# Performance work log

Measured on AMD Instinct MI355X. Metric: run time of the kernel, lower is better.

The kernel has to match this reference:

```python
import jax, jax.numpy as jnp
import numpy as np


def setup_inputs() -> dict:
    key = jax.random.key(0)
    k1, k2 = jax.random.split(key, 2)
    B, C, N, O, K = 4, 3, 8192, 64, 20
    x = jax.random.normal(k1, (B, C, N), dtype=jnp.float32)          # point cloud [B,3,N]
    W = jax.random.normal(k2, (O, 2 * C), dtype=jnp.float32) * 0.1   # 1x1 conv weight on 2C edge features
    b = jnp.zeros((O,), dtype=jnp.float32)
    return {"x": x, "W": W, "b": b, "k": K}


def _knn_idx(x, k):
    # x: [B, C, N]. Same math as torch knn(): pd = -||xi||^2 + 2 xi.xj - ||xj||^2,
    # topk of pd (largest) == k nearest neighbors.
    inner = -2.0 * jnp.einsum('bcn,bcm->bnm', x, x)      # [B,N,N]
    xx = jnp.sum(x * x, axis=1)                          # [B,N]
    pd = -xx[:, :, None] - inner - xx[:, None, :]        # [B,N,N] negative sq-dist
    _, idx = jax.lax.top_k(pd, k)                        # [B,N,k]
    return idx


def reference(x, W, b, k):
    # Faithful jax version of knn + get_graph_feature + 1x1 conv + LeakyReLU + max over k
    # (DGCNN EdgeConv layer, the hot path of the encoder).
    B, C, N = x.shape
    idx = _knn_idx(x, k)                                  # [B,N,k]
    xt = jnp.transpose(x, (0, 2, 1))                      # [B,N,C]
    nb = xt[jnp.arange(B)[:, None, None], idx]            # gather neighbors [B,N,k,C]
    cen = xt[:, :, None, :]                               # [B,N,1,C]
    feat = jnp.concatenate(
        [nb - cen, jnp.broadcast_to(cen, (B, N, k, C))], axis=-1)  # [B,N,k,2C]
    h = jnp.einsum('bnkc,oc->bonk', feat, W) + b[None, :, None, None]  # [B,O,N,k]
    h = jax.nn.leaky_relu(h, negative_slope=0.2)
    return jnp.max(h, axis=-1)                            # [B,O,N]
```

## Files before the change

### kernel.cpp

```cpp
#include <hip/hip_runtime.h>
#include <cstdint>
#include <climits>

#pragma clang fp contract(off)

#define N_PTS 8192
#define B_SZ  4
#define K_NN  20
#define O_CH  64
#define QW    64
#define SSUB  8
#define JSUB  (N_PTS / SSUB)
#define WARM  64
#define CAP   16
#define SPAD  17

typedef unsigned long long u64k;

__device__ __forceinline__ float pd_np(float qx, float qy, float qz, float xxn,
                                       float cx, float cy, float cz, float xm) {
  float p0 = qx * cx;
  float p1 = qy * cy;
  float p2 = qz * cz;
  float dot = (p0 + p1) + p2;
  float t = 2.0f * dot - xxn;
  return t - xm;
}

__device__ __forceinline__ void insert20(float (&arr)[K_NN], float v) {
  float c = v;
#pragma unroll
  for (int u = K_NN - 1; u >= 0; --u) {
    float hi = fmaxf(arr[u], c);
    c = fminf(arr[u], c);
    arr[u] = hi;
  }
}

__device__ __forceinline__ void insK(u64k (&a)[K_NN], u64k k) {
  u64k c = k;
#pragma unroll
  for (int u = K_NN - 1; u >= 0; --u) {
    bool g = a[u] > c;
    u64k hi = g ? a[u] : c;
    u64k lo = g ? c : a[u];
    a[u] = hi;
    c = lo;
  }
}

__device__ __forceinline__ u64k packKey(float pd, int j) {
  unsigned s = __float_as_uint(pd);
  unsigned sp = s ^ ((unsigned)((int)s >> 31) | 0x80000000u);
  return ((u64k)sp << 13) | (unsigned)(8191 - j);
}

__device__ __forceinline__ float keyPd(u64k k) {
  unsigned sp = (unsigned)(k >> 13);
  unsigned s = (sp & 0x80000000u) ? (sp & 0x7FFFFFFFu) : ~sp;
  return __uint_as_float(s);
}

__global__ __launch_bounds__(256, 2)
void pack_kernel(const float* __restrict__ x, float4* __restrict__ P) {
  int idx = blockIdx.x * 256 + threadIdx.x;
  if (idx >= B_SZ * N_PTS) return;
  int b = idx >> 13;
  int n = idx & (N_PTS - 1);
  const float* xb = x + (size_t)b * 3 * N_PTS;
  float x0 = xb[n];
  float x1 = xb[n + N_PTS];
  float x2 = xb[n + 2 * N_PTS];
  float xxv = (x0 * x0 + x1 * x1) + x2 * x2;
  P[idx] = make_float4(x0, x1, x2, xxv);
}

__global__ __launch_bounds__(512, 4)
void knn_edgeconv_kernel(const float4* __restrict__ P,
                         const float* __restrict__ W,
                         const float* __restrict__ bias,
                         float* __restrict__ out) {
  __shared__ u64k  stk[512 * SPAD];
  __shared__ float tau_l[QW];
  __shared__ int   cnt_l[512];
  __shared__ short of_l[512];
  __shared__ int   list_l[QW][21];

  const int t  = threadIdx.x;
  const int ql = t & 63;
  const int s  = t >> 6;
  const int wb = blockIdx.x;
  const int b  = wb >> 7;
  const int n0 = (wb & 127) << 6;
  const int q  = n0 + ql;

  const float4* __restrict__ Pb = P + (size_t)b * N_PTS;

  const float4 qc = Pb[q];
  const float qx = qc.x, qy = qc.y, qz = qc.z, xxn = qc.w;

  const int j0 = __builtin_amdgcn_readfirstlane(s) * JSUB;
  const bool is_owner = (t < QW);

  float arr[K_NN];
#pragma unroll
  for (int i = 0; i < K_NN; ++i) arr[i] = -__builtin_inff();
#pragma unroll 4
  for (int jj = 0; jj < WARM; ++jj) {
    int j = j0 + jj;
    float4 cd = Pb[j];
    float pd = pd_np(qx, qy, qz, xxn, cd.x, cd.y, cd.z, cd.w);
    if (pd > arr[0]) insert20(arr, pd);
  }
  {
    float* WV = (float*)stk;
#pragma unroll
    for (int i = 0; i < K_NN; ++i) WV[t * 21 + i] = arr[i];
  }
  __syncthreads();

  u64k karr[K_NN];
#pragma unroll
  for (int i = 0; i < K_NN; ++i) karr[i] = 0ULL;
  if (is_owner) {
    const float* WV = (const float*)stk;
#pragma unroll
    for (int p = 1; p < SSUB; ++p) {
      const float* pv = WV + ((p << 6) + t) * 21;
      for (int i = 0; i < K_NN; ++i) {
        float v = pv[i];
        if (v > arr[0]) insert20(arr, v);
      }
    }
    tau_l[t] = arr[0];
  }
  __syncthreads();

  const int CB[5] = {0, 128, 320, 640, 1024};
#pragma unroll
  for (int c = 0; c < 4; ++c) {
    const float tau = tau_l[ql];
    int cnt = 0;
    int ofj = -1;
    const int jb = j0 + CB[c];
    const int je = j0 + CB[c + 1];
#pragma unroll 4
    for (int j = jb; j < je; ++j) {
      float4 cd = Pb[j];
      float pd = pd_np(qx, qy, qz, xxn, cd.x, cd.y, cd.z, cd.w);
      if (pd >= tau) {
        if (cnt < CAP) {
          stk[t * SPAD + cnt] = packKey(pd, j);
          ++cnt;
        } else if (ofj < 0) {
          ofj = j;
        }
      }
    }
    cnt_l[t] = cnt;
    of_l[t]  = (short)ofj;
    __syncthreads();

    if (is_owner) {
#pragma unroll
      for (int p = 0; p < SSUB; ++p) {
        int pt = (p << 6) + t;
        int pc = cnt_l[pt];
        const u64k* ps = &stk[pt * SPAD];
        for (int i = 0; i < pc; ++i) {
          u64k k = ps[i];
          if (k > karr[0]) insK(karr, k);
        }
      }
#pragma unroll
      for (int p = 0; p < SSUB; ++p) {
        int pt = (p << 6) + t;
        int oj = of_l[pt];
        if (oj >= 0) {
          int pe = p * JSUB + CB[c + 1];
          for (int j = oj; j < pe; ++j) {
            float4 cd = Pb[j];
            float pdv = pd_np(qx, qy, qz, xxn, cd.x, cd.y, cd.z, cd.w);
            if (pdv >= tau) {
              u64k k = packKey(pdv, j);
              if (k > karr[0]) insK(karr, k);
            }
          }
        }
      }
      float t20 = keyPd(karr[0]);
      tau_l[t] = fmaxf(tau, t20);
    }
    __syncthreads();
  }

  if (is_owner) {
#pragma unroll
    for (int i = 0; i < K_NN; ++i)
      list_l[t][i] = 8191 - (int)(karr[i] & 8191ULL);
  }
  __syncthreads();

  float acc[8];
#pragma unroll
  for (int oi = 0; oi < 8; ++oi) acc[oi] = -__builtin_inff();
  const int o0 = s * 8;
  const float* __restrict__ Wp = W + o0 * 6;

  for (int nb = 0; nb < K_NN; ++nb) {
    int m = list_l[ql][nb] & (N_PTS - 1);
    float4 cm = Pb[m];
    float dx = cm.x - qx;
    float dy = cm.y - qy;
    float dz = cm.z - qz;
#pragma unroll
    for (int oi = 0; oi < 8; ++oi) {
      float h = __builtin_fmaf(dz, Wp[oi * 6 + 2],
                __builtin_fmaf(dy, Wp[oi * 6 + 1], dx * Wp[oi * 6 + 0]));
      acc[oi] = fmaxf(acc[oi], h);
    }
  }

#pragma unroll
  for (int oi = 0; oi < 8; ++oi) {
    int o = o0 + oi;
    float base = __builtin_fmaf(qz, Wp[oi * 6 + 5],
                 __builtin_fmaf(qy, Wp[oi * 6 + 4], qx * Wp[oi * 6 + 3])) + bias[o];
    float v = acc[oi] + base;
    v = fmaxf(v, 0.2f * v);
    out[((size_t)(b * O_CH + o) << 13) + q] = v;
  }
}

extern "C" void kernel_launch(void* const* d_in, const int* in_sizes, int n_in,
                              void* d_out, int out_size, void* d_ws, size_t ws_size,
                              hipStream_t stream) {
  const float* x    = (const float*)d_in[0];
  const float* W    = (const float*)d_in[1];
  const float* bias = (const float*)d_in[2];
  float4* P  = (float4*)d_ws;
  float* out = (float*)d_out;

  pack_kernel<<<dim3((B_SZ * N_PTS + 255) / 256), dim3(256), 0, stream>>>(x, P);
  knn_edgeconv_kernel<<<dim3(B_SZ * (N_PTS / QW)), dim3(512), 0, stream>>>(P, W, bias, out);
}
```

Before: 357.4 us.

## Dedicate one warp to merging while seven warps scan candidates, double-buffered

Splits the block so wave 0 only merges candidate keys into the top-20 while waves 1-7 scan 1170-point slices. Candidate buffers are double-buffered per chunk, so each scan chunk overlaps the merge of the previous one. The chunk schedule goes to six stages, CAP shrinks to 8, and the inner scan is manually unrolled by four. In exchange one wave no longer scans, there is one more barrier stage, and the smaller CAP may trigger more overflow rescans on the owner wave. The distance expression also now uses an fma, which may change rounding and therefore tie-breaking in neighbour selection.

```diff
diff --git a/kernel.cpp b/kernel.cpp
--- a/kernel.cpp
+++ b/kernel.cpp
@@ -9,11 +9,12 @@
 #define K_NN  20
 #define O_CH  64
 #define QW    64
-#define SSUB  8
-#define JSUB  (N_PTS / SSUB)
-#define WARM  64
-#define CAP   16
-#define SPAD  17
+#define NSW   7
+#define SUBL  1170
+#define WARM  96
+#define CAP   8
+#define SPAD  9
+#define NCH   6
 
 typedef unsigned long long u64k;
 
@@ -23,7 +24,7 @@
   float p1 = qy * cy;
   float p2 = qz * cz;
   float dot = (p0 + p1) + p2;
-  float t = 2.0f * dot - xxn;
+  float t = __builtin_fmaf(dot, 2.0f, -xxn);
   return t - xm;
 }
 
@@ -49,10 +50,13 @@
   }
 }
 
+__device__ __forceinline__ unsigned sortable32(float pd) {
+  unsigned s = __float_as_uint(pd);
+  return s ^ ((unsigned)((int)s >> 31) | 0x80000000u);
+}
+
 __device__ __forceinline__ u64k packKey(float pd, int j) {
-  unsigned s = __float_as_uint(pd);
-  unsigned sp = s ^ ((unsigned)((int)s >> 31) | 0x80000000u);
-  return ((u64k)sp << 13) | (unsigned)(8191 - j);
+  return ((u64k)sortable32(pd) << 13) | (unsigned)(8191 - j);
 }
 
 __device__ __forceinline__ float keyPd(u64k k) {
@@ -80,10 +84,10 @@
                          const float* __restrict__ W,
                          const float* __restrict__ bias,
                          float* __restrict__ out) {
-  __shared__ u64k  stk[512 * SPAD];
+  __shared__ u64k  stk[2 * NSW * 64 * SPAD];
+  __shared__ int   cnt2[2][NSW * 64];
+  __shared__ short of2[2][NSW * 64];
   __shared__ float tau_l[QW];
-  __shared__ int   cnt_l[512];
-  __shared__ short of_l[512];
   __shared__ int   list_l[QW][21];
 
   const int t  = threadIdx.x;
@@ -99,89 +103,105 @@
   const float4 qc = Pb[q];
   const float qx = qc.x, qy = qc.y, qz = qc.z, xxn = qc.w;
 
-  const int j0 = __builtin_amdgcn_readfirstlane(s) * JSUB;
-  const bool is_owner = (t < QW);
-
-  float arr[K_NN];
-#pragma unroll
-  for (int i = 0; i < K_NN; ++i) arr[i] = -__builtin_inff();
-#pragma unroll 4
-  for (int jj = 0; jj < WARM; ++jj) {
-    int j = j0 + jj;
-    float4 cd = Pb[j];
-    float pd = pd_np(qx, qy, qz, xxn, cd.x, cd.y, cd.z, cd.w);
-    if (pd > arr[0]) insert20(arr, pd);
-  }
-  {
+  const int sw   = __builtin_amdgcn_readfirstlane(s);
+  const int j0   = (sw - 1) * SUBL;
+  const int LEN  = (sw == 7) ? (N_PTS - 6 * SUBL) : SUBL;
+  const int tid7 = ((sw - 1) << 6) | ql;
+  const int CB[NCH + 1] = {0, 96, 192, 320, 512, 800, SUBL};
+
+  float arrv[K_NN];
+#pragma unroll
+  for (int i = 0; i < K_NN; ++i) arrv[i] = -__builtin_inff();
+  if (s >= 1) {
+    for (int jj = 0; jj < WARM; ++jj) {
+      int j = j0 + jj;
+      float4 cd = Pb[j];
+      float pd = pd_np(qx, qy, qz, xxn, cd.x, cd.y, cd.z, cd.w);
+      if (pd > arrv[0]) insert20(arrv, pd);
+    }
     float* WV = (float*)stk;
 #pragma unroll
-    for (int i = 0; i < K_NN; ++i) WV[t * 21 + i] = arr[i];
+    for (int i = 0; i < K_NN; ++i) WV[tid7 * 21 + i] = arrv[i];
   }
   __syncthreads();
 
   u64k karr[K_NN];
 #pragma unroll
   for (int i = 0; i < K_NN; ++i) karr[i] = 0ULL;
-  if (is_owner) {
+  if (s == 0) {
     const float* WV = (const float*)stk;
-#pragma unroll
-    for (int p = 1; p < SSUB; ++p) {
+    for (int p = 0; p < NSW; ++p) {
       const float* pv = WV + ((p << 6) + t) * 21;
       for (int i = 0; i < K_NN; ++i) {
         float v = pv[i];
-        if (v > arr[0]) insert20(arr, v);
-      }
-    }
-    tau_l[t] = arr[0];
+        if (v > arrv[0]) insert20(arrv, v);
+      }
+    }
+    tau_l[t] = arrv[0];
   }
   __syncthreads();
 
-  const int CB[5] = {0, 128, 320, 640, 1024};
-#pragma unroll
-  for (int c = 0; c < 4; ++c) {
-    const float tau = tau_l[ql];
-    int cnt = 0;
-    int ofj = -1;
-    const int jb = j0 + CB[c];
-    const int je = j0 + CB[c + 1];
-#pragma unroll 4
-    for (int j = jb; j < je; ++j) {
-      float4 cd = Pb[j];
-      float pd = pd_np(qx, qy, qz, xxn, cd.x, cd.y, cd.z, cd.w);
-      if (pd >= tau) {
-        if (cnt < CAP) {
-          stk[t * SPAD + cnt] = packKey(pd, j);
-          ++cnt;
-        } else if (ofj < 0) {
-          ofj = j;
-        }
-      }
-    }
-    cnt_l[t] = cnt;
-    of_l[t]  = (short)ofj;
-    __syncthreads();
-
-    if (is_owner) {
-#pragma unroll
-      for (int p = 0; p < SSUB; ++p) {
-        int pt = (p << 6) + t;
-        int pc = cnt_l[pt];
-        const u64k* ps = &stk[pt * SPAD];
+#define PUSH(pdv, jv)                                          \
+  if ((pdv) >= tau) {                                          \
+    if (cnt < CAP) { my[cnt] = packKey((pdv), (jv)); ++cnt; }  \
+    else if (ofj < 0) ofj = (jv);                              \
+  }
+
+  for (int st = 0; st <= NCH; ++st) {
+    if (s >= 1 && st < NCH) {
+      const int c = st;
+      const float tau = tau_l[ql];
+      int cnt = 0, ofj = -1;
+      const int jb = j0 + CB[c];
+      const int je = j0 + ((c == NCH - 1) ? LEN : CB[c + 1]);
+      u64k* my = stk + (size_t)(c & 1) * (NSW * 64 * SPAD) + (size_t)tid7 * SPAD;
+      int j = jb;
+      for (; j + 3 < je; j += 4) {
+        float4 d0 = Pb[j];
+        float4 d1 = Pb[j + 1];
+        float4 d2 = Pb[j + 2];
+        float4 d3 = Pb[j + 3];
+        float pd0 = pd_np(qx, qy, qz, xxn, d0.x, d0.y, d0.z, d0.w);
+        float pd1 = pd_np(qx, qy, qz, xxn, d1.x, d1.y, d1.z, d1.w);
+        float pd2 = pd_np(qx, qy, qz, xxn, d2.x, d2.y, d2.z, d2.w);
+        float pd3 = pd_np(qx, qy, qz, xxn, d3.x, d3.y, d3.z, d3.w);
+        PUSH(pd0, j)
+        PUSH(pd1, j + 1)
+        PUSH(pd2, j + 2)
+        PUSH(pd3, j + 3)
+      }
+      for (; j < je; ++j) {
+        float4 d0 = Pb[j];
+        float pd0 = pd_np(qx, qy, qz, xxn, d0.x, d0.y, d0.z, d0.w);
+        PUSH(pd0, j)
+      }
+      cnt2[c & 1][tid7] = cnt;
+      of2[c & 1][tid7]  = (short)ofj;
+    }
+    if (s == 0 && st >= 1) {
+      const int c = st - 1;
+      const float tauc = tau_l[t];
+      const u64k* sb = stk + (size_t)(c & 1) * (NSW * 64 * SPAD);
+      for (int p = 0; p < NSW; ++p) {
+        const int pt = (p << 6) + t;
+        int pc = cnt2[c & 1][pt];
+        const u64k* ps = sb + (size_t)pt * SPAD;
         for (int i = 0; i < pc; ++i) {
           u64k k = ps[i];
           if (k > karr[0]) insK(karr, k);
         }
       }
-#pragma unroll
-      for (int p = 0; p < SSUB; ++p) {
-        int pt = (p << 6) + t;
-        int oj = of_l[pt];
+      for (int p = 0; p < NSW; ++p) {
+        const int pt = (p << 6) + t;
+        int oj = of2[c & 1][pt];
         if (oj >= 0) {
-          int pe = p * JSUB + CB[c + 1];
-          for (int j = oj; j < pe; ++j) {
+          int je_abs = p * SUBL +
+              ((c == NCH - 1) ? ((p == NSW - 1) ? (N_PTS - 6 * SUBL) : SUBL)
+                              : CB[c + 1]);
+          for (int j = oj; j < je_abs; ++j) {
             float4 cd = Pb[j];
             float pdv = pd_np(qx, qy, qz, xxn, cd.x, cd.y, cd.z, cd.w);
-            if (pdv >= tau) {
+            if (pdv >= tauc) {
               u64k k = packKey(pdv, j);
               if (k > karr[0]) insK(karr, k);
             }
@@ -189,12 +209,13 @@
         }
       }
       float t20 = keyPd(karr[0]);
-      tau_l[t] = fmaxf(tau, t20);
+      tau_l[t] = fmaxf(tauc, t20);
     }
     __syncthreads();
   }
-
-  if (is_owner) {
+#undef PUSH
+
+  if (s == 0) {
 #pragma unroll
     for (int i = 0; i < K_NN; ++i)
       list_l[t][i] = 8191 - (int)(karr[i] & 8191ULL);
```

Measured after the change: 355.4 us. About the same (-0.5%).

## Transpose kNN scan so lanes own candidates and collect hits via shared atomics

Applied to the files above, without the earlier changes.

The candidate scan is restructured. Each lane now owns one candidate point and loops over all 64 block queries. Query coordinates come from broadcast loads, and each query's threshold is obtained with readlane. Hits are appended to per-query shared-memory lists through atomicAdd, replacing the per-thread fixed-capacity stacks and overflow offsets. Chunks become larger (5 chunks over the full point set), the merge spreads 8 queries per wave across 8 lanes, and a single-lane full rescan handles list overflow. The pd computation now uses an fma, which may change rounding and tie behaviour, and the serial overflow path could be costly if a list fills.

```diff
diff --git a/kernel.cpp b/kernel.cpp
--- a/kernel.cpp
+++ b/kernel.cpp
@@ -1,6 +1,5 @@
 #include <hip/hip_runtime.h>
 #include <cstdint>
-#include <climits>
 
 #pragma clang fp contract(off)
 
@@ -9,11 +8,11 @@
 #define K_NN  20
 #define O_CH  64
 #define QW    64
-#define SSUB  8
-#define JSUB  (N_PTS / SSUB)
+#define NWAVE 8
 #define WARM  64
-#define CAP   16
-#define SPAD  17
+#define CAPQ  56
+#define SPADQ 57
+#define NCH   5
 
 typedef unsigned long long u64k;
 
@@ -23,7 +22,7 @@
   float p1 = qy * cy;
   float p2 = qz * cz;
   float dot = (p0 + p1) + p2;
-  float t = 2.0f * dot - xxn;
+  float t = __builtin_fmaf(dot, 2.0f, -xxn);
   return t - xm;
 }
 
@@ -49,10 +48,13 @@
   }
 }
 
+__device__ __forceinline__ unsigned sortable32(float pd) {
+  unsigned s = __float_as_uint(pd);
+  return s ^ ((unsigned)((int)s >> 31) | 0x80000000u);
+}
+
 __device__ __forceinline__ u64k packKey(float pd, int j) {
-  unsigned s = __float_as_uint(pd);
-  unsigned sp = s ^ ((unsigned)((int)s >> 31) | 0x80000000u);
-  return ((u64k)sp << 13) | (unsigned)(8191 - j);
+  return ((u64k)sortable32(pd) << 13) | (unsigned)(8191 - j);
 }
 
 __device__ __forceinline__ float keyPd(u64k k) {
@@ -80,10 +82,9 @@
                          const float* __restrict__ W,
                          const float* __restrict__ bias,
                          float* __restrict__ out) {
-  __shared__ u64k  stk[512 * SPAD];
+  __shared__ u64k  smem[5376];
   __shared__ float tau_l[QW];
-  __shared__ int   cnt_l[512];
-  __shared__ short of_l[512];
+  __shared__ int   cnt_l[QW];
   __shared__ int   list_l[QW][21];
 
   const int t  = threadIdx.x;
@@ -95,109 +96,112 @@
   const int q  = n0 + ql;
 
   const float4* __restrict__ Pb = P + (size_t)b * N_PTS;
+  const float4* __restrict__ Pq = Pb + n0;
 
   const float4 qc = Pb[q];
   const float qx = qc.x, qy = qc.y, qz = qc.z, xxn = qc.w;
 
-  const int j0 = __builtin_amdgcn_readfirstlane(s) * JSUB;
-  const bool is_owner = (t < QW);
-
-  float arr[K_NN];
-#pragma unroll
-  for (int i = 0; i < K_NN; ++i) arr[i] = -__builtin_inff();
-#pragma unroll 4
-  for (int jj = 0; jj < WARM; ++jj) {
-    int j = j0 + jj;
-    float4 cd = Pb[j];
-    float pd = pd_np(qx, qy, qz, xxn, cd.x, cd.y, cd.z, cd.w);
-    if (pd > arr[0]) insert20(arr, pd);
-  }
+  const int sw  = __builtin_amdgcn_readfirstlane(s);
+  const int myq = (sw << 3) + ql;
+
+  float arrv[K_NN];
+#pragma unroll
+  for (int i = 0; i < K_NN; ++i) arrv[i] = -__builtin_inff();
   {
-    float* WV = (float*)stk;
-#pragma unroll
-    for (int i = 0; i < K_NN; ++i) WV[t * 21 + i] = arr[i];
+    const int jb = sw * WARM;
+    for (int jj = 0; jj < WARM; ++jj) {
+      float4 cd = Pb[jb + jj];
+      float pdv = pd_np(qx, qy, qz, xxn, cd.x, cd.y, cd.z, cd.w);
+      if (pdv > arrv[0]) insert20(arrv, pdv);
+    }
+    float* WV = (float*)smem;
+#pragma unroll
+    for (int i = 0; i < K_NN; ++i) WV[t * 21 + i] = arrv[i];
   }
   __syncthreads();
 
   u64k karr[K_NN];
 #pragma unroll
   for (int i = 0; i < K_NN; ++i) karr[i] = 0ULL;
-  if (is_owner) {
-    const float* WV = (const float*)stk;
-#pragma unroll
-    for (int p = 1; p < SSUB; ++p) {
-      const float* pv = WV + ((p << 6) + t) * 21;
+  if (ql < 8) {
+    const float* WV = (const float*)smem;
+    float m[K_NN];
+#pragma unroll
+    for (int i = 0; i < K_NN; ++i) m[i] = -__builtin_inff();
+    for (int p = 0; p < NWAVE; ++p) {
+      const float* pv = WV + ((p << 6) + myq) * 21;
       for (int i = 0; i < K_NN; ++i) {
         float v = pv[i];
-        if (v > arr[0]) insert20(arr, v);
+        if (v > m[0]) insert20(m, v);
       }
     }
-    tau_l[t] = arr[0];
+    tau_l[myq] = m[0];
+    cnt_l[myq] = 0;
   }
   __syncthreads();
 
-  const int CB[5] = {0, 128, 320, 640, 1024};
-#pragma unroll
-  for (int c = 0; c < 4; ++c) {
-    const float tau = tau_l[ql];
-    int cnt = 0;
-    int ofj = -1;
-    const int jb = j0 + CB[c];
-    const int je = j0 + CB[c + 1];
+  const int CB[NCH + 1] = {0, 512, 1024, 2048, 4096, 8192};
+  u64k* stk = smem;
+
+  for (int c = 0; c < NCH; ++c) {
+    {
+      const int csz  = CB[c + 1] - CB[c];
+      const int nbat = csz >> 9;
+      const int jb   = CB[c] + sw * (csz >> 3);
+      const int tau_own = __float_as_int(tau_l[ql]);
+      for (int bt = 0; bt < nbat; ++bt) {
+        const int j = jb + (bt << 6) + ql;
+        const float4 cd = Pb[j];
+        const float cx = cd.x, cy = cd.y, cz = cd.z, cw = cd.w;
 #pragma unroll 4
-    for (int j = jb; j < je; ++j) {
-      float4 cd = Pb[j];
-      float pd = pd_np(qx, qy, qz, xxn, cd.x, cd.y, cd.z, cd.w);
-      if (pd >= tau) {
-        if (cnt < CAP) {
-          stk[t * SPAD + cnt] = packKey(pd, j);
-          ++cnt;
-        } else if (ofj < 0) {
-          ofj = j;
-        }
-      }
-    }
-    cnt_l[t] = cnt;
-    of_l[t]  = (short)ofj;
-    __syncthreads();
-
-    if (is_owner) {
-#pragma unroll
-      for (int p = 0; p < SSUB; ++p) {
-        int pt = (p << 6) + t;
-        int pc = cnt_l[pt];
-        const u64k* ps = &stk[pt * SPAD];
-        for (int i = 0; i < pc; ++i) {
-          u64k k = ps[i];
-          if (k > karr[0]) insK(karr, k);
-        }
-      }
-#pragma unroll
-      for (int p = 0; p < SSUB; ++p) {
-        int pt = (p << 6) + t;
-        int oj = of_l[pt];
-        if (oj >= 0) {
-          int pe = p * JSUB + CB[c + 1];
-          for (int j = oj; j < pe; ++j) {
-            float4 cd = Pb[j];
-            float pdv = pd_np(qx, qy, qz, xxn, cd.x, cd.y, cd.z, cd.w);
-            if (pdv >= tau) {
-              u64k k = packKey(pdv, j);
-              if (k > karr[0]) insK(karr, k);
-            }
+        for (int qi = 0; qi < QW; ++qi) {
+          const float4 qv = Pq[qi];
+          const float stau = __int_as_float(__builtin_amdgcn_readlane(tau_own, qi));
+          float pdv = pd_np(qv.x, qv.y, qv.z, qv.w, cx, cy, cz, cw);
+          if (pdv >= stau) {
+            int slot = atomicAdd(&cnt_l[qi], 1);
+            if (slot < CAPQ)
+              stk[qi * SPADQ + slot] =
+                  ((u64k)__float_as_uint(pdv) << 32) | (unsigned)j;
           }
         }
       }
+    }
+    __syncthreads();
+
+    if (ql < 8) {
+      const float tauc = tau_l[myq];
+      const int pc = cnt_l[myq];
+      if (pc <= CAPQ) {
+        for (int i = 0; i < pc; ++i) {
+          u64k e = stk[myq * SPADQ + i];
+          float pdv = __uint_as_float((unsigned)(e >> 32));
+          int jv = (int)(e & 0xFFFFFFFFu);
+          u64k k = packKey(pdv, jv);
+          if (k > karr[0]) insK(karr, k);
+        }
+      } else {
+        float4 mq = Pq[myq];
+        for (int j = CB[c]; j < CB[c + 1]; ++j) {
+          float4 cd = Pb[j];
+          float pdv = pd_np(mq.x, mq.y, mq.z, mq.w, cd.x, cd.y, cd.z, cd.w);
+          if (pdv >= tauc) {
+            u64k k = packKey(pdv, j);
+            if (k > karr[0]) insK(karr, k);
+          }
+        }
+      }
+      cnt_l[myq] = 0;
       float t20 = keyPd(karr[0]);
-      tau_l[t] = fmaxf(tau, t20);
+      tau_l[myq] = fmaxf(tauc, t20);
     }
     __syncthreads();
   }
 
-  if (is_owner) {
+  if (ql < 8) {
 #pragma unroll
     for (int i = 0; i < K_NN; ++i)
-      list_l[t][i] = 8191 - (int)(karr[i] & 8191ULL);
+      list_l[myq][i] = 8191 - (int)(karr[i] & 8191ULL);
   }
   __syncthreads();
 
```

After: 402.0 us. 1.12x slower.

## Split candidate scan across 16 sub-ranges with 1024-thread blocks

Applied to the files above, without the earlier changes.

Doubles the number of threads per query group from 8 to 16 by splitting the N candidates into 16 slices, shrinking per-thread scan length and per-thread candidate stack (CAP 7). The warm-up threshold merge is done in two shared-memory rounds to fit the reduced buffer, and the EdgeConv output is split 4 channels per thread. The aim is more parallelism and latency hiding in the brute-force distance scan. In exchange, the single owner thread per query has twice as many partial lists to merge, with more overflow rescans and more barriers. It also uses an FMA in the distance formula, which can change rounding relative to the reference.

```diff
diff --git a/kernel.cpp b/kernel.cpp
--- a/kernel.cpp
+++ b/kernel.cpp
@@ -1,6 +1,5 @@
 #include <hip/hip_runtime.h>
 #include <cstdint>
-#include <climits>
 
 #pragma clang fp contract(off)
 
@@ -9,11 +8,13 @@
 #define K_NN  20
 #define O_CH  64
 #define QW    64
-#define SSUB  8
-#define JSUB  (N_PTS / SSUB)
+#define SSUB  16
+#define NTHR  (QW * SSUB)
+#define SUBL  (N_PTS / SSUB)
 #define WARM  64
-#define CAP   16
-#define SPAD  17
+#define CAP   7
+#define SPAD  8
+#define NCH   4
 
 typedef unsigned long long u64k;
 
@@ -23,7 +24,7 @@
   float p1 = qy * cy;
   float p2 = qz * cz;
   float dot = (p0 + p1) + p2;
-  float t = 2.0f * dot - xxn;
+  float t = __builtin_fmaf(dot, 2.0f, -xxn);
   return t - xm;
 }
 
@@ -49,10 +50,13 @@
   }
 }
 
+__device__ __forceinline__ unsigned sortable32(float pd) {
+  unsigned s = __float_as_uint(pd);
+  return s ^ ((unsigned)((int)s >> 31) | 0x80000000u);
+}
+
 __device__ __forceinline__ u64k packKey(float pd, int j) {
-  unsigned s = __float_as_uint(pd);
-  unsigned sp = s ^ ((unsigned)((int)s >> 31) | 0x80000000u);
-  return ((u64k)sp << 13) | (unsigned)(8191 - j);
+  return ((u64k)sortable32(pd) << 13) | (unsigned)(8191 - j);
 }
 
 __device__ __forceinline__ float keyPd(u64k k) {
@@ -75,15 +79,15 @@
   P[idx] = make_float4(x0, x1, x2, xxv);
 }
 
-__global__ __launch_bounds__(512, 4)
+__global__ __launch_bounds__(NTHR, 8)
 void knn_edgeconv_kernel(const float4* __restrict__ P,
                          const float* __restrict__ W,
                          const float* __restrict__ bias,
                          float* __restrict__ out) {
-  __shared__ u64k  stk[512 * SPAD];
+  __shared__ u64k  stk[NTHR * SPAD];
+  __shared__ int   cnt_l[NTHR];
+  __shared__ short of_l[NTHR];
   __shared__ float tau_l[QW];
-  __shared__ int   cnt_l[512];
-  __shared__ short of_l[512];
   __shared__ int   list_l[QW][21];
 
   const int t  = threadIdx.x;
@@ -99,89 +103,104 @@
   const float4 qc = Pb[q];
   const float qx = qc.x, qy = qc.y, qz = qc.z, xxn = qc.w;
 
-  const int j0 = __builtin_amdgcn_readfirstlane(s) * JSUB;
-  const bool is_owner = (t < QW);
-
-  float arr[K_NN];
-#pragma unroll
-  for (int i = 0; i < K_NN; ++i) arr[i] = -__builtin_inff();
+  const int sw   = __builtin_amdgcn_readfirstlane(s);
+  const int j0   = sw * SUBL;
+  const int CB[NCH + 1] = {0, 64, 160, 320, 512};
+
+  float arrv[K_NN];
+#pragma unroll
+  for (int i = 0; i < K_NN; ++i) arrv[i] = -__builtin_inff();
 #pragma unroll 4
   for (int jj = 0; jj < WARM; ++jj) {
     int j = j0 + jj;
     float4 cd = Pb[j];
-    float pd = pd_np(qx, qy, qz, xxn, cd.x, cd.y, cd.z, cd.w);
-    if (pd > arr[0]) insert20(arr, pd);
-  }
+    float pdv = pd_np(qx, qy, qz, xxn, cd.x, cd.y, cd.z, cd.w);
+    if (pdv > arrv[0]) insert20(arrv, pdv);
+  }
+
+  float mreg[K_NN];
+#pragma unroll
+  for (int i = 0; i < K_NN; ++i) mreg[i] = -__builtin_inff();
   {
     float* WV = (float*)stk;
-#pragma unroll
-    for (int i = 0; i < K_NN; ++i) WV[t * 21 + i] = arr[i];
+    if (sw < 8) {
+#pragma unroll
+      for (int i = 0; i < K_NN; ++i) WV[((sw << 6) + ql) * 21 + i] = arrv[i];
+    }
+    __syncthreads();
+    if (t < QW) {
+      for (int p = 0; p < 8; ++p) {
+        const float* pv = WV + ((p << 6) + t) * 21;
+        for (int i = 0; i < K_NN; ++i) {
+          float v = pv[i];
+          if (v > mreg[0]) insert20(mreg, v);
+        }
+      }
+    }
+    __syncthreads();
+    if (sw >= 8) {
+#pragma unroll
+      for (int i = 0; i < K_NN; ++i) WV[(((sw - 8) << 6) + ql) * 21 + i] = arrv[i];
+    }
+    __syncthreads();
+    if (t < QW) {
+      for (int p = 0; p < 8; ++p) {
+        const float* pv = WV + ((p << 6) + t) * 21;
+        for (int i = 0; i < K_NN; ++i) {
+          float v = pv[i];
+          if (v > mreg[0]) insert20(mreg, v);
+        }
+      }
+      tau_l[t] = mreg[0];
+    }
   }
   __syncthreads();
 
   u64k karr[K_NN];
 #pragma unroll
   for (int i = 0; i < K_NN; ++i) karr[i] = 0ULL;
-  if (is_owner) {
-    const float* WV = (const float*)stk;
-#pragma unroll
-    for (int p = 1; p < SSUB; ++p) {
-      const float* pv = WV + ((p << 6) + t) * 21;
-      for (int i = 0; i < K_NN; ++i) {
-        float v = pv[i];
-        if (v > arr[0]) insert20(arr, v);
-      }
-    }
-    tau_l[t] = arr[0];
-  }
-  __syncthreads();
-
-  const int CB[5] = {0, 128, 320, 640, 1024};
-#pragma unroll
-  for (int c = 0; c < 4; ++c) {
-    const float tau = tau_l[ql];
-    int cnt = 0;
-    int ofj = -1;
-    const int jb = j0 + CB[c];
-    const int je = j0 + CB[c + 1];
+
+  for (int c = 0; c < NCH; ++c) {
+    {
+      const float tau = tau_l[ql];
+      int cnt = 0, ofj = -1;
+      const int jb = j0 + CB[c];
+      const int je = j0 + CB[c + 1];
+      u64k* my = stk + (size_t)t * SPAD;
 #pragma unroll 4
-    for (int j = jb; j < je; ++j) {
-      float4 cd = Pb[j];
-      float pd = pd_np(qx, qy, qz, xxn, cd.x, cd.y, cd.z, cd.w);
-      if (pd >= tau) {
-        if (cnt < CAP) {
-          stk[t * SPAD + cnt] = packKey(pd, j);
-          ++cnt;
-        } else if (ofj < 0) {
-          ofj = j;
-        }
-      }
-    }
-    cnt_l[t] = cnt;
-    of_l[t]  = (short)ofj;
-    __syncthreads();
-
-    if (is_owner) {
-#pragma unroll
+      for (int j = jb; j < je; ++j) {
+        float4 cd = Pb[j];
+        float pdv = pd_np(qx, qy, qz, xxn, cd.x, cd.y, cd.z, cd.w);
+        if (pdv >= tau) {
+          if (cnt < CAP) { my[cnt] = packKey(pdv, j); ++cnt; }
+          else if (ofj < 0) ofj = j;
+        }
+      }
+      cnt_l[t] = cnt;
+      of_l[t]  = (short)(ofj < 0 ? -1 : (ofj - j0));
+    }
+    __syncthreads();
+
+    if (t < QW) {
+      const float tauc = tau_l[t];
       for (int p = 0; p < SSUB; ++p) {
-        int pt = (p << 6) + t;
-        int pc = cnt_l[pt];
-        const u64k* ps = &stk[pt * SPAD];
+        const int pt = (p << 6) + t;
+        const int pc = cnt_l[pt];
+        const u64k* ps = stk + (size_t)pt * SPAD;
         for (int i = 0; i < pc; ++i) {
           u64k k = ps[i];
           if (k > karr[0]) insK(karr, k);
         }
       }
-#pragma unroll
       for (int p = 0; p < SSUB; ++p) {
-        int pt = (p << 6) + t;
+        const int pt = (p << 6) + t;
         int oj = of_l[pt];
         if (oj >= 0) {
-          int pe = p * JSUB + CB[c + 1];
-          for (int j = oj; j < pe; ++j) {
+          const int pb = p * SUBL;
+          for (int j = pb + oj; j < pb + CB[c + 1]; ++j) {
             float4 cd = Pb[j];
             float pdv = pd_np(qx, qy, qz, xxn, cd.x, cd.y, cd.z, cd.w);
-            if (pdv >= tau) {
+            if (pdv >= tauc) {
               u64k k = packKey(pdv, j);
               if (k > karr[0]) insK(karr, k);
             }
@@ -189,22 +208,22 @@
         }
       }
       float t20 = keyPd(karr[0]);
-      tau_l[t] = fmaxf(tau, t20);
-    }
-    __syncthreads();
-  }
-
-  if (is_owner) {
+      tau_l[t] = fmaxf(tauc, t20);
+    }
+    __syncthreads();
+  }
+
+  if (t < QW) {
 #pragma unroll
     for (int i = 0; i < K_NN; ++i)
       list_l[t][i] = 8191 - (int)(karr[i] & 8191ULL);
   }
   __syncthreads();
 
-  float acc[8];
-#pragma unroll
-  for (int oi = 0; oi < 8; ++oi) acc[oi] = -__builtin_inff();
-  const int o0 = s * 8;
+  float acc[4];
+#pragma unroll
+  for (int oi = 0; oi < 4; ++oi) acc[oi] = -__builtin_inff();
+  const int o0 = s * 4;
   const float* __restrict__ Wp = W + o0 * 6;
 
   for (int nb = 0; nb < K_NN; ++nb) {
@@ -214,7 +233,7 @@
     float dy = cm.y - qy;
     float dz = cm.z - qz;
 #pragma unroll
-    for (int oi = 0; oi < 8; ++oi) {
+    for (int oi = 0; oi < 4; ++oi) {
       float h = __builtin_fmaf(dz, Wp[oi * 6 + 2],
                 __builtin_fmaf(dy, Wp[oi * 6 + 1], dx * Wp[oi * 6 + 0]));
       acc[oi] = fmaxf(acc[oi], h);
@@ -222,7 +241,7 @@
   }
 
 #pragma unroll
-  for (int oi = 0; oi < 8; ++oi) {
+  for (int oi = 0; oi < 4; ++oi) {
     int o = o0 + oi;
     float base = __builtin_fmaf(qz, Wp[oi * 6 + 5],
                  __builtin_fmaf(qy, Wp[oi * 6 + 4], qx * Wp[oi * 6 + 3])) + bias[o];
@@ -242,5 +261,5 @@
   float* out = (float*)d_out;
 
   pack_kernel<<<dim3((B_SZ * N_PTS + 255) / 256), dim3(256), 0, stream>>>(x, P);
-  knn_edgeconv_kernel<<<dim3(B_SZ * (N_PTS / QW)), dim3(512), 0, stream>>>(P, W, bias, out);
-}
+  knn_edgeconv_kernel<<<dim3(B_SZ * (N_PTS / QW)), dim3(NTHR), 0, stream>>>(P, W, bias, out);
+}
```

Result: slower. 865.2 us (+142.1%).
